# Optimization experiments

Hardware: AMD Instinct MI355X
Metric: run time of the kernel (lower is better)

The kernel has to match this reference:

```python
import jax, jax.numpy as jnp
import numpy as np

W, H = 512, 512
SHIFT_NORM = 100.0
P = 1
WEIGHT = 10.0
EPS = 1e-16


def _cv_matrix(angle, scale, shift, cx, cy):
    # cv2.getRotationMatrix2D-style matrix (pixel coords) with extra x-shift.
    alpha = scale * jnp.cos(angle)
    beta = scale * jnp.sin(angle)
    row0 = jnp.stack([alpha, beta, (1.0 - alpha) * cx - beta * cy + shift], axis=-1)
    row1 = jnp.stack([-beta, alpha, beta * cx + (1.0 - alpha) * cy], axis=-1)
    return jnp.stack([row0, row1], axis=-2)  # [B,2,3]


def _normalize_transform(M, width, height):
    # Convert pixel-space affine to normalized [-1,1] coords (align_corners=True).
    a, b, tx = M[:, 0, 0], M[:, 0, 1], M[:, 0, 2]
    c, d, ty = M[:, 1, 0], M[:, 1, 1], M[:, 1, 2]
    sw = float(width - 1)
    sh = float(height - 1)
    A = a
    Bc = b * sh / sw
    Cc = a + b * sh / sw + 2.0 * tx / sw - 1.0
    D = c * sw / sh
    E = d
    Fc = c * sw / sh + d + 2.0 * ty / sh - 1.0
    row0 = jnp.stack([A, Bc, Cc], axis=-1)
    row1 = jnp.stack([D, E, Fc], axis=-1)
    return jnp.stack([row0, row1], axis=-2)  # [B,2,3]


def _affine_grid(T, height, width):
    # torch affine_grid, align_corners=True
    u = jnp.linspace(-1.0, 1.0, width, dtype=T.dtype)
    v = jnp.linspace(-1.0, 1.0, height, dtype=T.dtype)
    vv, uu = jnp.meshgrid(v, u, indexing='ij')
    base = jnp.stack([uu, vv, jnp.ones_like(uu)], axis=-1)  # [H,W,3]
    return jnp.einsum('bij,hwj->bhwi', T, base)  # [B,H,W,2] (x,y)


def _grid_sample(img, grid):
    # bilinear, zeros padding, align_corners=True. img [B,C,H,W], grid [B,Ho,Wo,2]
    B, C, Hi, Wi = img.shape
    x = (grid[..., 0] + 1.0) * (Wi - 1) / 2.0
    y = (grid[..., 1] + 1.0) * (Hi - 1) / 2.0
    x0 = jnp.floor(x)
    y0 = jnp.floor(y)
    wx1 = x - x0
    wy1 = y - y0
    wx0 = 1.0 - wx1
    wy0 = 1.0 - wy1

    def gather(xi, yi):
        valid = ((xi >= 0) & (xi < Wi) & (yi >= 0) & (yi < Hi)).astype(img.dtype)
        xc = jnp.clip(xi, 0, Wi - 1).astype(jnp.int32)
        yc = jnp.clip(yi, 0, Hi - 1).astype(jnp.int32)
        g = jax.vmap(lambda im, xb, yb, vb: im[:, yb, xb] * vb[None])
        return g(img, xc, yc, valid)  # [B,C,Ho,Wo]

    out = (gather(x0, y0) * (wx0 * wy0)[:, None]
           + gather(x0 + 1, y0) * (wx1 * wy0)[:, None]
           + gather(x0, y0 + 1) * (wx0 * wy1)[:, None]
           + gather(x0 + 1, y0 + 1) * (wx1 * wy1)[:, None])
    return out


def setup_inputs() -> dict:
    key = jax.random.key(0)
    k1, k2, k3 = jax.random.split(key, 3)
    theta = jax.random.normal(k1, (32, 3), dtype=jnp.float32)
    img_R = jax.random.normal(k2, (32, 3, H, W), dtype=jnp.float32)
    img_R_orig = jax.random.normal(k3, (32, 3, H, W), dtype=jnp.float32)
    return {"theta": theta, "img_R": img_R, "img_R_orig": img_R_orig}


def reference(theta, img_R, img_R_orig):
    cx, cy = W // 2, H // 2
    M = _cv_matrix(theta[:, 0], theta[:, 1], SHIFT_NORM * theta[:, 2], cx, cy)
    T = _normalize_transform(M, W, H)
    grid = _affine_grid(T, H, W)
    warped = _grid_sample(img_R_orig, grid)
    mask = jnp.ones((img_R.shape[0], 1, H, W), dtype=img_R.dtype)
    warped_mask = _grid_sample(mask, grid)[:, 0]  # [B,H,W]
    # p=1 norm over channel dim
    nrm = jnp.sum(jnp.abs(img_R - warped), axis=1)  # [B,H,W]
    num = jnp.sum(warped_mask * nrm, axis=(1, 2)) + EPS
    den = jnp.sum(warped_mask, axis=(1, 2)) + EPS
    losses = WEIGHT * num / den
    return jnp.mean(losses)
```

## Files before the change

kernel.cpp:

```cpp
#include <hip/hip_runtime.h>
#include <math.h>

#define IMG_W 512
#define IMG_H 512
#define NB 32
#define NC 3
#define PLANE (IMG_H * IMG_W)

#define TILE_W 32
#define TILE_H 32
#define TILES_X (IMG_W / TILE_W)
#define TILES_Y (IMG_H / TILE_H)
#define TILES_PER_B (TILES_X * TILES_Y)
#define NBLOCKS (NB * TILES_PER_B)

#define LDSF 6144

typedef float vfloat4 __attribute__((ext_vector_type(4)));


__global__ __launch_bounds__(256) void recon_main(
    const float* __restrict__ theta,
    const float* __restrict__ img_R,
    const float* __restrict__ img_orig,
    float* __restrict__ ws)
{
    __shared__ __align__(16) float tileLds[LDSF];
    __shared__ float snum[4];
    __shared__ float sden[4];

    const int lin = blockIdx.x;
    const int xcd = lin & 7;
    const int loc = lin >> 3;
    const int b   = xcd * 4 + (loc >> 8);
    const int tile = loc & 255;
    const int tx = (tile & (TILES_X - 1)) * TILE_W;
    const int ty = (tile >> 4) * TILE_H;

    const int tid  = threadIdx.x;
    const int trow = tid >> 3;
    const int tcol = (tid & 7) * 4;

    const float ang   = theta[b * 3 + 0];
    const float s     = theta[b * 3 + 1];
    const float shift = 100.0f * theta[b * 3 + 2];
    float sn, cs;
    sincosf(ang, &sn, &cs);
    const float alpha = s * cs;
    const float beta  = s * sn;
    const float tx_a = (1.0f - alpha) * 256.0f - beta * 256.0f + shift;
    const float ty_a = beta * 256.0f + (1.0f - alpha) * 256.0f;
    const float Cc = alpha + beta + 2.0f * tx_a / 511.0f - 1.0f;
    const float Fc = -beta + alpha + 2.0f * ty_a / 511.0f - 1.0f;
    const float X0 = 255.5f * (Cc + 1.0f - alpha - beta);
    const float Y0 = 255.5f * (Fc + 1.0f + beta - alpha);

    const float* orig_b = img_orig + (size_t)b * NC * PLANE;
    const float* R_b    = img_R    + (size_t)b * NC * PLANE;

    const int h  = ty + trow;
    const int w0 = tx + tcol;
    const int p0 = h * IMG_W + w0;

    const float xb = X0 + alpha * (float)w0 + beta * (float)h;
    const float yb = Y0 - beta * (float)w0 + alpha * (float)h;

    int   xi0a[4], xi1a[4], yi0a[4], yi1a[4];
    float w00[4], w10[4], w01[4], w11[4], mk[4];
    float den_acc = 0.0f;

#pragma unroll
    for (int j = 0; j < 4; ++j) {
        const float x = xb + alpha * (float)j;
        const float y = yb - beta  * (float)j;
        const float x0f = floorf(x), y0f = floorf(y);
        const float fx1 = x - x0f,  fy1 = y - y0f;
        const float fx0 = 1.0f - fx1, fy0 = 1.0f - fy1;
        const float vx0 = (x0f >=  0.0f && x0f <= 511.0f) ? 1.0f : 0.0f;
        const float vx1 = (x0f >= -1.0f && x0f <= 510.0f) ? 1.0f : 0.0f;
        const float vy0 = (y0f >=  0.0f && y0f <= 511.0f) ? 1.0f : 0.0f;
        const float vy1 = (y0f >= -1.0f && y0f <= 510.0f) ? 1.0f : 0.0f;
        xi0a[j] = (int)fminf(fmaxf(x0f,        0.0f), 511.0f);
        xi1a[j] = (int)fminf(fmaxf(x0f + 1.0f, 0.0f), 511.0f);
        yi0a[j] = (int)fminf(fmaxf(y0f,        0.0f), 511.0f);
        yi1a[j] = (int)fminf(fmaxf(y0f + 1.0f, 0.0f), 511.0f);
        w00[j] = fx0 * fy0 * vx0 * vy0;
        w10[j] = fx1 * fy0 * vx1 * vy0;
        w01[j] = fx0 * fy1 * vx0 * vy1;
        w11[j] = fx1 * fy1 * vx1 * vy1;
        mk[j]  = w00[j] + w10[j] + w01[j] + w11[j];
        den_acc += mk[j];
    }

    const float fx_lo = (float)tx, fx_hi = (float)(tx + TILE_W - 1);
    const float fy_lo = (float)ty, fy_hi = (float)(ty + TILE_H - 1);
    const float cxA = X0 + alpha * fx_lo + beta * fy_lo;
    const float cxB = X0 + alpha * fx_hi + beta * fy_lo;
    const float cxC = X0 + alpha * fx_lo + beta * fy_hi;
    const float cxD = X0 + alpha * fx_hi + beta * fy_hi;
    const float cyA = Y0 - beta * fx_lo + alpha * fy_lo;
    const float cyB = Y0 - beta * fx_hi + alpha * fy_lo;
    const float cyC = Y0 - beta * fx_lo + alpha * fy_hi;
    const float cyD = Y0 - beta * fx_hi + alpha * fy_hi;
    const float min_x = fminf(fminf(cxA, cxB), fminf(cxC, cxD));
    const float max_x = fmaxf(fmaxf(cxA, cxB), fmaxf(cxC, cxD));
    const float min_y = fminf(fminf(cyA, cyB), fminf(cyC, cyD));
    const float max_y = fmaxf(fmaxf(cyA, cyB), fmaxf(cyC, cyD));

    int xlo = (int)floorf(min_x);
    int xhi = (int)floorf(max_x) + 1;
    xlo = min(max(xlo, 0), 511);
    xhi = min(max(xhi, 0), 511);
    xlo &= ~3;
    int ylo = (int)floorf(min_y);
    int yhi = (int)floorf(max_y) + 1;
    ylo = min(max(ylo, 0), 511);
    yhi = min(max(yhi, 0), 511);

    const int bw = xhi - xlo + 1;
    const int bh = yhi - ylo + 1;
    int stride = (bw + 3) & ~3;
    if (((stride >> 2) & 1) == 0) stride += 4;
    const int nq4 = stride >> 2;
    const bool staged = (stride * bh <= LDSF) && (nq4 <= 32);

    float nrm[4] = {0.0f, 0.0f, 0.0f, 0.0f};

    if (staged) {
        int l00[4], l10[4], l01[4], l11[4];
#pragma unroll
        for (int j = 0; j < 4; ++j) {
            const int r0 = (yi0a[j] - ylo) * stride - xlo;
            const int r1 = (yi1a[j] - ylo) * stride - xlo;
            l00[j] = r0 + xi0a[j];
            l10[j] = r0 + xi1a[j];
            l01[j] = r1 + xi0a[j];
            l11[j] = r1 + xi1a[j];
        }
        const int qq  = tid & 31;
        const int r00 = tid >> 5;
        const int col = xlo + (qq << 2);
        const bool doload = (col <= xhi);

        for (int c = 0; c < NC; ++c) {
            if (c) __syncthreads();
            const float* plane = orig_b + c * PLANE;
            if (doload) {
                for (int r = r00; r < bh; r += 8) {
                    const vfloat4 v = *(const vfloat4*)(plane + (ylo + r) * IMG_W + col);
                    *(vfloat4*)(&tileLds[r * stride + (qq << 2)]) = v;
                }
            }
            __syncthreads();
            const vfloat4 rv = __builtin_nontemporal_load(
                                 (const vfloat4*)(R_b + c * PLANE + p0));
            const float rj[4] = {rv.x, rv.y, rv.z, rv.w};
#pragma unroll
            for (int j = 0; j < 4; ++j) {
                const float s00 = tileLds[l00[j]];
                const float s10 = tileLds[l10[j]];
                const float s01 = tileLds[l01[j]];
                const float s11 = tileLds[l11[j]];
                const float warped = s00 * w00[j] + s10 * w10[j]
                                   + s01 * w01[j] + s11 * w11[j];
                nrm[j] += fabsf(rj[j] - warped);
            }
        }
    } else {
        int a0[4], a1[4], sl0[4], sl1[4];
#pragma unroll
        for (int j = 0; j < 4; ++j) {
            const int xc = min(xi0a[j], 510);
            a0[j]  = yi0a[j] * IMG_W + xc;
            a1[j]  = yi1a[j] * IMG_W + xc;
            sl0[j] = xi0a[j] - xc;
            sl1[j] = xi1a[j] - xc;
        }
#pragma unroll
        for (int c = 0; c < NC; ++c) {
            const float* plane = orig_b + c * PLANE;
            const vfloat4 rv = __builtin_nontemporal_load(
                                 (const vfloat4*)(R_b + c * PLANE + p0));
            const float rj[4] = {rv.x, rv.y, rv.z, rv.w};
#pragma unroll
            for (int j = 0; j < 4; ++j) {
                const float2 t0 = *(const float2*)(plane + a0[j]);
                const float2 t1 = *(const float2*)(plane + a1[j]);
                const float s00 = sl0[j] ? t0.y : t0.x;
                const float s10 = sl1[j] ? t0.y : t0.x;
                const float s01 = sl0[j] ? t1.y : t1.x;
                const float s11 = sl1[j] ? t1.y : t1.x;
                const float warped = s00 * w00[j] + s10 * w10[j]
                                   + s01 * w01[j] + s11 * w11[j];
                nrm[j] += fabsf(rj[j] - warped);
            }
        }
    }

    float num_acc = 0.0f;
#pragma unroll
    for (int j = 0; j < 4; ++j) num_acc += mk[j] * nrm[j];

#pragma unroll
    for (int off = 32; off > 0; off >>= 1) {
        num_acc += __shfl_down(num_acc, off);
        den_acc += __shfl_down(den_acc, off);
    }

    const int wave = threadIdx.x >> 6;
    const int lane = threadIdx.x & 63;
    if (lane == 0) { snum[wave] = num_acc; sden[wave] = den_acc; }
    __syncthreads();
    if (threadIdx.x == 0) {
        ws[lin]           = snum[0] + snum[1] + snum[2] + snum[3];
        ws[NBLOCKS + lin] = sden[0] + sden[1] + sden[2] + sden[3];
    }
}

__global__ __launch_bounds__(256) void recon_final(
    const float* __restrict__ ws,
    float* __restrict__ out)
{
    __shared__ float sloss[NB];
    const int t = threadIdx.x;
    const int b = t >> 3;
    const int j = t & 7;

    float n = 0.0f, d = 0.0f;
    for (int k = 0; k < 32; ++k) {
        const int tile = j * 32 + k;
        const int lin  = ((b & 3) * 256 + tile) * 8 + (b >> 2);
        n += ws[lin];
        d += ws[NBLOCKS + lin];
    }
#pragma unroll
    for (int off = 4; off > 0; off >>= 1) {
        n += __shfl_down(n, off);
        d += __shfl_down(d, off);
    }
    if (j == 0) sloss[b] = 10.0f * (n + 1e-16f) / (d + 1e-16f);
    __syncthreads();
    if (t == 0) {
        float L = 0.0f;
#pragma unroll
        for (int i = 0; i < NB; ++i) L += sloss[i];
        out[0] = L * (1.0f / (float)NB);
    }
}

extern "C" void kernel_launch(void* const* d_in, const int* in_sizes, int n_in,
                              void* d_out, int out_size, void* d_ws, size_t ws_size,
                              hipStream_t stream) {
    const float* theta    = (const float*)d_in[0];
    const float* img_R    = (const float*)d_in[1];
    const float* img_orig = (const float*)d_in[2];
    float* out = (float*)d_out;
    float* ws  = (float*)d_ws;

    recon_main<<<NBLOCKS, 256, 0, stream>>>(theta, img_R, img_orig, ws);
    recon_final<<<1, 256, 0, stream>>>(ws, out);
}
```

Measured before the change: 253.8 us.

## Stage all three channels in LDS at once and prefetch img_R early

Stages all three channel tiles into separate LDS regions in a single pass with one barrier, replacing three per-channel load/sync phases. The img_R loads are issued at kernel start so they overlap with the transform math. The load thread mapping adapts to tile width, and the x+1 neighbour reads use a +1 offset with a select. LDS usage rises to about 48KB and occupancy is pinned at 3 blocks, while the per-channel staging capacity drops, so more tiles may take the uncached gather path.

New measurement: 227.0 us. 1.12x faster.

```diff
diff --git a/kernel.cpp b/kernel.cpp
--- a/kernel.cpp
+++ b/kernel.cpp
@@ -14,18 +14,19 @@
 #define TILES_PER_B (TILES_X * TILES_Y)
 #define NBLOCKS (NB * TILES_PER_B)
 
-#define LDSF 6144
+#define LDSC 4096
+#define LDSF (3 * LDSC)
 
 typedef float vfloat4 __attribute__((ext_vector_type(4)));
 
 
-__global__ __launch_bounds__(256) void recon_main(
+__global__ __launch_bounds__(256, 3) void recon_main(
     const float* __restrict__ theta,
     const float* __restrict__ img_R,
     const float* __restrict__ img_orig,
     float* __restrict__ ws)
 {
-    __shared__ __align__(16) float tileLds[LDSF];
+    __shared__ __align__(16) float tileLds[LDSF + 8];
     __shared__ float snum[4];
     __shared__ float sden[4];
 
@@ -40,6 +41,17 @@
     const int tid  = threadIdx.x;
     const int trow = tid >> 3;
     const int tcol = (tid & 7) * 4;
+
+    const int h  = ty + trow;
+    const int w0 = tx + tcol;
+    const int p0 = h * IMG_W + w0;
+
+    const float* orig_b = img_orig + (size_t)b * NC * PLANE;
+    const float* R_b    = img_R    + (size_t)b * NC * PLANE;
+
+    const vfloat4 rv0 = *(const vfloat4*)(R_b + 0 * PLANE + p0);
+    const vfloat4 rv1 = *(const vfloat4*)(R_b + 1 * PLANE + p0);
+    const vfloat4 rv2 = *(const vfloat4*)(R_b + 2 * PLANE + p0);
 
     const float ang   = theta[b * 3 + 0];
     const float s     = theta[b * 3 + 1];
@@ -54,13 +66,6 @@
     const float Fc = -beta + alpha + 2.0f * ty_a / 511.0f - 1.0f;
     const float X0 = 255.5f * (Cc + 1.0f - alpha - beta);
     const float Y0 = 255.5f * (Fc + 1.0f + beta - alpha);
-
-    const float* orig_b = img_orig + (size_t)b * NC * PLANE;
-    const float* R_b    = img_R    + (size_t)b * NC * PLANE;
-
-    const int h  = ty + trow;
-    const int w0 = tx + tcol;
-    const int p0 = h * IMG_W + w0;
 
     const float xb = X0 + alpha * (float)w0 + beta * (float)h;
     const float yb = Y0 - beta * (float)w0 + alpha * (float)h;
@@ -122,70 +127,73 @@
     int stride = (bw + 3) & ~3;
     if (((stride >> 2) & 1) == 0) stride += 4;
     const int nq4 = stride >> 2;
-    const bool staged = (stride * bh <= LDSF) && (nq4 <= 32);
+    const bool staged = (stride * bh <= LDSC) && (nq4 <= 32);
 
     float nrm[4] = {0.0f, 0.0f, 0.0f, 0.0f};
 
     if (staged) {
-        int l00[4], l10[4], l01[4], l11[4];
+        int l00[4], l01[4], u0x[4];
 #pragma unroll
         for (int j = 0; j < 4; ++j) {
             const int r0 = (yi0a[j] - ylo) * stride - xlo;
             const int r1 = (yi1a[j] - ylo) * stride - xlo;
             l00[j] = r0 + xi0a[j];
-            l10[j] = r0 + xi1a[j];
             l01[j] = r1 + xi0a[j];
-            l11[j] = r1 + xi1a[j];
-        }
-        const int qq  = tid & 31;
-        const int r00 = tid >> 5;
+            u0x[j] = xi1a[j] - xi0a[j];
+        }
+        int qq, r00, rstep;
+        if (nq4 <= 8)       { qq = tid & 7;  r00 = tid >> 3; rstep = 32; }
+        else if (nq4 <= 16) { qq = tid & 15; r00 = tid >> 4; rstep = 16; }
+        else                { qq = tid & 31; r00 = tid >> 5; rstep = 8;  }
         const int col = xlo + (qq << 2);
-        const bool doload = (col <= xhi);
-
+        if (col <= xhi) {
+            for (int r = r00; r < bh; r += rstep) {
+                const float* src = orig_b + (ylo + r) * IMG_W + col;
+                float* dst = &tileLds[r * stride + (qq << 2)];
+#pragma unroll
+                for (int c = 0; c < NC; ++c)
+                    *(vfloat4*)(dst + c * LDSC) = *(const vfloat4*)(src + c * PLANE);
+            }
+        }
+        __syncthreads();
+
+#pragma unroll
         for (int c = 0; c < NC; ++c) {
-            if (c) __syncthreads();
-            const float* plane = orig_b + c * PLANE;
-            if (doload) {
-                for (int r = r00; r < bh; r += 8) {
-                    const vfloat4 v = *(const vfloat4*)(plane + (ylo + r) * IMG_W + col);
-                    *(vfloat4*)(&tileLds[r * stride + (qq << 2)]) = v;
-                }
-            }
-            __syncthreads();
-            const vfloat4 rv = __builtin_nontemporal_load(
-                                 (const vfloat4*)(R_b + c * PLANE + p0));
+            const vfloat4 rv = (c == 0) ? rv0 : (c == 1) ? rv1 : rv2;
             const float rj[4] = {rv.x, rv.y, rv.z, rv.w};
+            const float* buf = &tileLds[c * LDSC];
 #pragma unroll
             for (int j = 0; j < 4; ++j) {
-                const float s00 = tileLds[l00[j]];
-                const float s10 = tileLds[l10[j]];
-                const float s01 = tileLds[l01[j]];
-                const float s11 = tileLds[l11[j]];
-                const float warped = s00 * w00[j] + s10 * w10[j]
-                                   + s01 * w01[j] + s11 * w11[j];
+                const float a0 = buf[l00[j]];
+                const float a1 = buf[l00[j] + 1];
+                const float b0 = buf[l01[j]];
+                const float b1 = buf[l01[j] + 1];
+                const float s10 = u0x[j] ? a1 : a0;
+                const float s11 = u0x[j] ? b1 : b0;
+                const float warped = a0 * w00[j] + s10 * w10[j]
+                                   + b0 * w01[j] + s11 * w11[j];
                 nrm[j] += fabsf(rj[j] - warped);
             }
         }
     } else {
-        int a0[4], a1[4], sl0[4], sl1[4];
+        int a0i[4], a1i[4], sl0[4], sl1[4];
 #pragma unroll
         for (int j = 0; j < 4; ++j) {
             const int xc = min(xi0a[j], 510);
-            a0[j]  = yi0a[j] * IMG_W + xc;
-            a1[j]  = yi1a[j] * IMG_W + xc;
+            a0i[j] = yi0a[j] * IMG_W + xc;
+            a1i[j] = yi1a[j] * IMG_W + xc;
             sl0[j] = xi0a[j] - xc;
             sl1[j] = xi1a[j] - xc;
         }
 #pragma unroll
         for (int c = 0; c < NC; ++c) {
             const float* plane = orig_b + c * PLANE;
-            const vfloat4 rv = __builtin_nontemporal_load(
-                                 (const vfloat4*)(R_b + c * PLANE + p0));
+            const vfloat4 rv = (c == 0) ? rv0 : (c == 1) ? rv1 : rv2;
             const float rj[4] = {rv.x, rv.y, rv.z, rv.w};
 #pragma unroll
             for (int j = 0; j < 4; ++j) {
-                const float2 t0 = *(const float2*)(plane + a0[j]);
-                const float2 t1 = *(const float2*)(plane + a1[j]);
+                const float2 t0 = *(const float2*)(plane + a0i[j]);
+                const float2 t1 = *(const float2*)(plane + a1i[j]);
                 const float s00 = sl0[j] ? t0.y : t0.x;
                 const float s10 = sl1[j] ? t0.y : t0.x;
                 const float s01 = sl0[j] ? t1.y : t1.x;
```
